# Kernel optimization log

Measured on AMD Instinct MI355X. Metric: run time of the kernel, lower is better.

## Reference

```python
import jax, jax.numpy as jnp
import numpy as np

B, H, D, SIZE, S = 32, 16, 64, 262144, 1024
GAMMA = 0.99

def setup_inputs() -> dict:
    key = jax.random.key(0)
    k1, k2, k3, k4 = jax.random.split(key, 4)
    return {
        "query": jax.random.normal(k1, (B, H, D), jnp.float32),
        "key_store": jax.random.normal(k2, (SIZE, H, D), jnp.float32),
        "value_store": jax.random.normal(k3, (SIZE, H, D), jnp.float32),
        "logit_store": 0.1 * jax.random.normal(k4, (SIZE, H), jnp.float32),
    }

def _sample_indices(logit_store, batch, rng):
    # torch softmax over dim=0 (batch*head rows) => per-row weights over s are
    # w[s] proportional to exp(logit[s,h]) / sum_h' exp(logit[s,h'])
    logw = logit_store.T - jax.nn.logsumexp(logit_store, axis=1)[None, :]  # (H, SIZE)
    u = jax.random.uniform(rng, (batch,) + logw.shape, minval=1e-12, maxval=1.0)
    gumbel = -jnp.log(-jnp.log(u))
    # Gumbel top-k == sampling without replacement proportional to exp(logw)
    _, idx = jax.lax.top_k(logw[None] + gumbel, S)  # (B, H, S)
    return idx

def reference(query, key_store, value_store, logit_store):
    b, h, d = query.shape
    idx = _sample_indices(logit_store, b, jax.random.key(42))  # (B,H,S)
    hidx = jnp.arange(h)[None, :, None]  # (1,H,1) broadcasts against idx
    kst = key_store.transpose(1, 0, 2)   # (H, SIZE, D)
    vst = value_store.transpose(1, 0, 2)
    sk = kst[hidx, idx]  # (B,H,S,D) gathered sample keys
    sv = vst[hidx, idx]  # (B,H,S,D) gathered sample values
    attn = jax.nn.softmax(jnp.einsum('bhd,bhsd->bhs', query, sk) * (d ** -0.5), axis=-1)
    lerp_k = jnp.einsum('bhs,bhsd->bhd', attn, sk)
    lerp_v = jnp.einsum('bhs,bhsd->bhd', attn, sv)
    # scattered in-place store updates
    new_k = (1.0 - attn)[..., None] * sk + attn[..., None] * lerp_k[:, :, None, :]
    new_v = (1.0 - attn)[..., None] * sv + attn[..., None] * lerp_v[:, :, None, :]
    key_store_new = kst.at[hidx, idx].set(new_k).transpose(1, 0, 2)
    value_store_new = vst.at[hidx, idx].set(new_v).transpose(1, 0, 2)
    lst = logit_store.T  # (H, SIZE)
    new_l = GAMMA * lst[hidx, idx] + attn  # RHS uses gathered old logits (matches torch)
    logit_store_new = lst.at[hidx, idx].set(new_l).T
    return lerp_k, lerp_v, key_store_new, value_store_new, logit_store_new
```

## Files before the change

kernel.cpp:

```cpp
#include <hip/hip_runtime.h>
#include <stdint.h>

static constexpr int NB = 32, NH = 16, ND = 64, NS = 1024;
static constexpr int SZ = 262144;
static constexpr int NROW = NB * NH;
static constexpr long N4 = 67108864L;
static constexpr long HALF4 = 33554432L;
static constexpr int SPLIT_IDX = 131072;

typedef float f32x4 __attribute__((ext_vector_type(4)));

__device__ __forceinline__ uint32_t rotl32(uint32_t x, int r) { return (x << r) | (x >> (32 - r)); }

__device__ __forceinline__ void tf2x32(uint32_t x0, uint32_t x1, uint32_t& o0, uint32_t& o1) {
  const uint32_t K1 = 42u, K2 = 0x1BD11BF0u;
  x1 += K1;
#define TFR(r) { x0 += x1; x1 = rotl32(x1, (r)); x1 ^= x0; }
  TFR(13) TFR(15) TFR(26) TFR(6)
  x0 += K1; x1 += K2 + 1u;
  TFR(17) TFR(29) TFR(16) TFR(24)
  x0 += K2; x1 += 2u;
  TFR(13) TFR(15) TFR(26) TFR(6)
  x1 += K1 + 3u;
  TFR(17) TFR(29) TFR(16) TFR(24)
  x0 += K1; x1 += K2 + 4u;
  TFR(13) TFR(15) TFR(26) TFR(6)
  x0 += K2; x1 += 5u;
#undef TFR
  o0 = x0; o1 = x1;
}

__device__ __forceinline__ uint32_t bits_of(uint32_t row, uint32_t s) {
  uint32_t o0, o1; tf2x32(0u, (row << 18) | s, o0, o1);
  return o0 ^ o1;
}

__device__ __forceinline__ float gumbel_precise(uint32_t row, uint32_t s) {
  uint32_t bits = bits_of(row, s);
  float f = __uint_as_float((bits >> 9) | 0x3f800000u) - 1.0f;
  float u = fmaxf(1e-12f, f + 1e-12f);
  float t = -logf(u);
  return -logf(t);
}

__device__ __forceinline__ float uf_of(uint32_t row, uint32_t s) {
  return __uint_as_float((bits_of(row, s) >> 9) | 0x3f800000u);
}

__device__ __forceinline__ uint32_t fkey(float v) {
  uint32_t u = __float_as_uint(v);
  return (u & 0x80000000u) ? ~u : (u | 0x80000000u);
}

__global__ void k_logw(const float* __restrict__ logit, float* __restrict__ logw,
                       float* __restrict__ wexp, float* __restrict__ outL,
                       int* __restrict__ winner, float* __restrict__ W) {
  __shared__ float sW[16];
  const int tid = threadIdx.x;
  if (tid < 16) sW[tid] = 0.f;
  __syncthreads();
  int s = blockIdx.x * 256 + tid;
  const float4* p = (const float4*)(logit + (size_t)s * NH);
  float4 a0 = p[0], a1 = p[1], a2 = p[2], a3 = p[3];
  float x[16] = {a0.x,a0.y,a0.z,a0.w, a1.x,a1.y,a1.z,a1.w,
                 a2.x,a2.y,a2.z,a2.w, a3.x,a3.y,a3.z,a3.w};
  float m = x[0];
#pragma unroll
  for (int h = 1; h < 16; ++h) m = fmaxf(m, x[h]);
  float acc = 0.f;
#pragma unroll
  for (int h = 0; h < 16; ++h) acc += expf(x[h] - m);
  float lse = logf(acc) + m;
  float wl[16];
#pragma unroll
  for (int h = 0; h < 16; ++h) {
    float lw = x[h] - lse;
    logw[(size_t)h * SZ + s] = lw;
    float e = expf(lw);
    wexp[(size_t)h * SZ + s] = e;
    wl[h] = e;
  }
#pragma unroll
  for (int h = 0; h < 16; ++h) {
    float v = wl[h];
#pragma unroll
    for (int off = 32; off; off >>= 1) v += __shfl_xor(v, off);
    if ((tid & 63) == 0) atomicAdd(&sW[h], v);
  }
  float4* q = (float4*)(outL + (size_t)s * NH);
  q[0] = a0; q[1] = a1; q[2] = a2; q[3] = a3;
  int4 mone = make_int4(-1, -1, -1, -1);
  int4* w = (int4*)(winner + (size_t)s * NH);
  w[0] = mone; w[1] = mone; w[2] = mone; w[3] = mone;
  __syncthreads();
  if (tid < 16) atomicAdd(&W[tid], sW[tid]);
}

__device__ __forceinline__ void find_thresh(const uint32_t* hist, int nbins, int chunk,
                                            uint32_t need, int* outT, int tid) {
  if (tid < 64) {
    int hi = nbins - 1 - tid * chunk;
    uint32_t csum = 0;
    for (int j = 0; j < chunk; ++j) csum += hist[hi - j];
    uint32_t inc = csum;
#pragma unroll
    for (int off = 1; off < 64; off <<= 1) {
      uint32_t t = (uint32_t)__shfl_up((int)inc, off);
      if (tid >= off) inc += t;
    }
    uint32_t pre = inc - csum;
    if (pre < need && inc >= need) {
      uint32_t cum = pre; int T = hi - chunk + 1;
      for (int j = 0; j < chunk; ++j) {
        int b = hi - j;
        if (cum + hist[b] >= need) { T = b; break; }
        cum += hist[b];
      }
      *outT = T;
    }
  }
}

#define MEGA_T 512
#define SEL_BLKS 512
#define COPY_BLKS 2048
#define NCAND 5120
__global__ void __launch_bounds__(MEGA_T, 8) k_mega(
    const float* __restrict__ logw, const float* __restrict__ wexp,
    const float* __restrict__ Wsum, const float* __restrict__ qin,
    const float* __restrict__ Kst, const float* __restrict__ Vst,
    int* __restrict__ idx_sel, float* __restrict__ attn_ws,
    float* __restrict__ lerp_k, float* __restrict__ lerp_v, int* __restrict__ winner,
    f32x4* __restrict__ oK4, f32x4* __restrict__ oV4) {
  const int bid = blockIdx.x;
  const int tid = threadIdx.x;

  if (bid >= SEL_BLKS) {
    const f32x4* K4 = (const f32x4*)Kst;
    const f32x4* V4 = (const f32x4*)Vst;
    const long base = (long)(bid - SEL_BLKS) * MEGA_T + tid;
    const long stride = (long)COPY_BLKS * MEGA_T;
    for (int r = 0; r < 8; ++r) {
      long i0 = base + (long)(4 * r) * stride;
      long i1 = i0 + stride, i2 = i0 + 2 * stride, i3 = i0 + 3 * stride;
      f32x4 k0 = __builtin_nontemporal_load(&K4[i0]);
      f32x4 k1 = __builtin_nontemporal_load(&K4[i1]);
      f32x4 k2 = __builtin_nontemporal_load(&K4[i2]);
      f32x4 k3 = __builtin_nontemporal_load(&K4[i3]);
      f32x4 v0 = __builtin_nontemporal_load(&V4[i0]);
      f32x4 v1 = __builtin_nontemporal_load(&V4[i1]);
      f32x4 v2 = __builtin_nontemporal_load(&V4[i2]);
      f32x4 v3 = __builtin_nontemporal_load(&V4[i3]);
      __builtin_nontemporal_store(k0, &oK4[i0]);
      __builtin_nontemporal_store(k1, &oK4[i1]);
      __builtin_nontemporal_store(k2, &oK4[i2]);
      __builtin_nontemporal_store(k3, &oK4[i3]);
      __builtin_nontemporal_store(v0, &oV4[i0]);
      __builtin_nontemporal_store(v1, &oV4[i1]);
      __builtin_nontemporal_store(v2, &oV4[i2]);
      __builtin_nontemporal_store(v3, &oV4[i3]);
    }
    return;
  }

  const int row = bid;
  const int h = row & 15, b = row >> 4;
  const float* lw = logw + (size_t)h * SZ;
  const f32x4* we4 = (const f32x4*)(wexp + (size_t)h * SZ);
  int* outrow = idx_sel + (size_t)row * NS;

  __shared__ union {
    struct {
      int      cidx[NCAND];
      uint32_t hist[2048];
      uint16_t candA[2048];
      uint16_t candB[256];
      uint16_t candC[64];
    } s;
    struct {
      int   sel_s[NS];
      float sc[NS];
      float red[MEGA_T];
      f32x4 pk4[8][16], pv4[8][16];
    } a;
  } u;
  __shared__ int ctl[8];
  __shared__ float sNB;

  if (tid == 0) {
    float Wh = Wsum[h];
    sNB = -4096.0f / Wh;
    ctl[1] = 0;
  }
  __syncthreads();
  const float nB = sNB;
  const float CThr = 1.9999996f;

  for (int g = tid; g < SZ / 4; g += MEGA_T) {
    f32x4 w4 = we4[g];
    int s0 = g << 2;
    float u0 = uf_of(row, s0);
    float u1 = uf_of(row, s0 + 1);
    float u2 = uf_of(row, s0 + 2);
    float u3 = uf_of(row, s0 + 3);
    if (u0 >= fmaf(nB, w4.x, CThr)) { int p = atomicAdd(&ctl[1], 1); if (p < NCAND) u.s.cidx[p] = s0; }
    if (u1 >= fmaf(nB, w4.y, CThr)) { int p = atomicAdd(&ctl[1], 1); if (p < NCAND) u.s.cidx[p] = s0 + 1; }
    if (u2 >= fmaf(nB, w4.z, CThr)) { int p = atomicAdd(&ctl[1], 1); if (p < NCAND) u.s.cidx[p] = s0 + 2; }
    if (u3 >= fmaf(nB, w4.w, CThr)) { int p = atomicAdd(&ctl[1], 1); if (p < NCAND) u.s.cidx[p] = s0 + 3; }
  }
  __syncthreads();
  const int C = min(ctl[1], NCAND);

  for (int i = tid; i < 2048; i += MEGA_T) u.s.hist[i] = 0;
  if (tid == 0) { ctl[0] = 0; ctl[3] = 0; ctl[4] = 0; ctl[5] = 0; }
  __syncthreads();
  for (int ci = tid; ci < C; ci += MEGA_T) {
    int s = u.s.cidx[ci];
    uint32_t k = fkey(lw[s] + gumbel_precise(row, s));
    atomicAdd(&u.s.hist[k >> 21], 1u);
  }
  __syncthreads();
  find_thresh(u.s.hist, 2048, 32, (uint32_t)NS, &ctl[2], tid);
  __syncthreads();
  const int T0 = ctl[2];
  for (int ci = tid; ci < C; ci += MEGA_T) {
    int s = u.s.cidx[ci];
    uint32_t k = fkey(lw[s] + gumbel_precise(row, s));
    int bb = (int)(k >> 21);
    if (bb > T0)       { int p = atomicAdd(&ctl[0], 1); outrow[p] = s; }
    else if (bb == T0) { int c = atomicAdd(&ctl[3], 1); if (c < 2048) u.s.candA[c] = (uint16_t)ci; }
  }
  __syncthreads();
  const int CA = min(ctl[3], 2048);
  for (int i = tid; i < 2048; i += MEGA_T) u.s.hist[i] = 0;
  __syncthreads();
  for (int i = tid; i < CA; i += MEGA_T) {
    int s = u.s.cidx[u.s.candA[i]];
    uint32_t k = fkey(lw[s] + gumbel_precise(row, s));
    atomicAdd(&u.s.hist[(k >> 10) & 0x7FFu], 1u);
  }
  __syncthreads();
  find_thresh(u.s.hist, 2048, 32, (uint32_t)(NS - ctl[0]), &ctl[2], tid);
  __syncthreads();
  const int T1 = ctl[2];
  for (int i = tid; i < CA; i += MEGA_T) {
    int ci = u.s.candA[i];
    int s = u.s.cidx[ci];
    uint32_t k = fkey(lw[s] + gumbel_precise(row, s));
    int mid = (int)((k >> 10) & 0x7FFu);
    if (mid > T1)       { int p = atomicAdd(&ctl[0], 1); outrow[p] = s; }
    else if (mid == T1) { int c = atomicAdd(&ctl[4], 1); if (c < 256) u.s.candB[c] = (uint16_t)ci; }
  }
  __syncthreads();
  const int CB = min(ctl[4], 256);
  for (int i = tid; i < 1024; i += MEGA_T) u.s.hist[i] = 0;
  __syncthreads();
  for (int i = tid; i < CB; i += MEGA_T) {
    int s = u.s.cidx[u.s.candB[i]];
    uint32_t k = fkey(lw[s] + gumbel_precise(row, s));
    atomicAdd(&u.s.hist[k & 0x3FFu], 1u);
  }
  __syncthreads();
  find_thresh(u.s.hist, 1024, 16, (uint32_t)(NS - ctl[0]), &ctl[2], tid);
  __syncthreads();
  const int T2 = ctl[2];
  for (int i = tid; i < CB; i += MEGA_T) {
    int ci = u.s.candB[i];
    int s = u.s.cidx[ci];
    uint32_t k = fkey(lw[s] + gumbel_precise(row, s));
    int lo = (int)(k & 0x3FFu);
    if (lo > T2)       { int p = atomicAdd(&ctl[0], 1); outrow[p] = s; }
    else if (lo == T2) { int c = atomicAdd(&ctl[5], 1); if (c < 64) u.s.candC[c] = (uint16_t)ci; }
  }
  __syncthreads();
  if (tid == 0) {
    int need = NS - ctl[0];
    int cc = min(ctl[5], 64);
    for (int k = 0; k < need; ++k) {
      int best = 0x7fffffff, bi = 0;
      for (int j = 0; j < cc; ++j) { int s = u.s.cidx[u.s.candC[j]]; if (s < best) { best = s; bi = j; } }
      if (best == 0x7fffffff) best = 0;
      outrow[ctl[0] + k] = best;
      if (cc > 0) u.s.cidx[u.s.candC[bi]] = 0x7fffffff;
    }
  }
  __syncthreads();

  const f32x4* K4 = (const f32x4*)Kst;
  const f32x4* V4 = (const f32x4*)Vst;
  const int lane = tid & 63, wv = tid >> 6;
  const int sj = lane >> 3, dj = lane & 7;
  for (int i = tid; i < NS; i += MEGA_T) u.a.sel_s[i] = outrow[i];
  const f32x4* q4 = (const f32x4*)(qin + (size_t)row * ND);
  f32x4 qa = q4[dj * 2], qb = q4[dj * 2 + 1];
  __syncthreads();
  for (int it = 0; it < 16; it += 2) {
    int i1 = it * 64 + wv * 8 + sj;
    int i2 = i1 + 64;
    int x1 = u.a.sel_s[i1], x2 = u.a.sel_s[i2];
    size_t b1 = ((size_t)x1 * NH + h) * 16 + dj * 2;
    size_t b2 = ((size_t)x2 * NH + h) * 16 + dj * 2;
    f32x4 ka1 = K4[b1], kb1 = K4[b1 + 1];
    f32x4 ka2 = K4[b2], kb2 = K4[b2 + 1];
    float p1 = ka1.x*qa.x + ka1.y*qa.y + ka1.z*qa.z + ka1.w*qa.w
             + kb1.x*qb.x + kb1.y*qb.y + kb1.z*qb.z + kb1.w*qb.w;
    float p2 = ka2.x*qa.x + ka2.y*qa.y + ka2.z*qa.z + ka2.w*qa.w
             + kb2.x*qb.x + kb2.y*qb.y + kb2.z*qb.z + kb2.w*qb.w;
#pragma unroll
    for (int off = 1; off < 8; off <<= 1) { p1 += __shfl_xor(p1, off); p2 += __shfl_xor(p2, off); }
    if (dj == 0) { u.a.sc[i1] = p1 * 0.125f; u.a.sc[i2] = p2 * 0.125f; }
  }
  __syncthreads();
  float v1 = u.a.sc[tid], v2 = u.a.sc[tid + 512];
  u.a.red[tid] = fmaxf(v1, v2); __syncthreads();
  for (int s = 256; s; s >>= 1) { if (tid < s) u.a.red[tid] = fmaxf(u.a.red[tid], u.a.red[tid + s]); __syncthreads(); }
  float m = u.a.red[0]; __syncthreads();
  float e1 = expf(v1 - m), e2 = expf(v2 - m);
  u.a.red[tid] = e1 + e2; __syncthreads();
  for (int s = 256; s; s >>= 1) { if (tid < s) u.a.red[tid] += u.a.red[tid + s]; __syncthreads(); }
  float inv = 1.0f / u.a.red[0];
  float a1 = e1 * inv, a2 = e2 * inv;
  u.a.sc[tid] = a1; u.a.sc[tid + 512] = a2;
  attn_ws[(size_t)row * NS + tid] = a1;
  attn_ws[(size_t)row * NS + tid + 512] = a2;
  __syncthreads();
  f32x4 AK = 0.f, BK = 0.f, AV = 0.f, BV = 0.f;
  for (int it = 0; it < 16; it += 2) {
    int i1 = it * 64 + wv * 8 + sj;
    int i2 = i1 + 64;
    int x1 = u.a.sel_s[i1], x2 = u.a.sel_s[i2];
    float c1 = u.a.sc[i1], c2 = u.a.sc[i2];
    size_t b1 = ((size_t)x1 * NH + h) * 16 + dj * 2;
    size_t b2 = ((size_t)x2 * NH + h) * 16 + dj * 2;
    f32x4 k1a = K4[b1], k1b = K4[b1 + 1], v1a = V4[b1], v1b = V4[b1 + 1];
    f32x4 k2a = K4[b2], k2b = K4[b2 + 1], v2a = V4[b2], v2b = V4[b2 + 1];
    AK += c1 * k1a + c2 * k2a; BK += c1 * k1b + c2 * k2b;
    AV += c1 * v1a + c2 * v2a; BV += c1 * v1b + c2 * v2b;
  }
#pragma unroll
  for (int off = 8; off < 64; off <<= 1) {
    AK.x += __shfl_xor(AK.x, off); AK.y += __shfl_xor(AK.y, off);
    AK.z += __shfl_xor(AK.z, off); AK.w += __shfl_xor(AK.w, off);
    BK.x += __shfl_xor(BK.x, off); BK.y += __shfl_xor(BK.y, off);
    BK.z += __shfl_xor(BK.z, off); BK.w += __shfl_xor(BK.w, off);
    AV.x += __shfl_xor(AV.x, off); AV.y += __shfl_xor(AV.y, off);
    AV.z += __shfl_xor(AV.z, off); AV.w += __shfl_xor(AV.w, off);
    BV.x += __shfl_xor(BV.x, off); BV.y += __shfl_xor(BV.y, off);
    BV.z += __shfl_xor(BV.z, off); BV.w += __shfl_xor(BV.w, off);
  }
  if (sj == 0) {
    u.a.pk4[wv][dj * 2] = AK; u.a.pk4[wv][dj * 2 + 1] = BK;
    u.a.pv4[wv][dj * 2] = AV; u.a.pv4[wv][dj * 2 + 1] = BV;
  }
  __syncthreads();
  if (tid < 64) {
    float lk = 0.f, lv = 0.f;
    const float* pkf = (const float*)u.a.pk4;
    const float* pvf = (const float*)u.a.pv4;
#pragma unroll
    for (int ww = 0; ww < 8; ++ww) { lk += pkf[ww * 64 + tid]; lv += pvf[ww * 64 + tid]; }
    lerp_k[(size_t)row * ND + tid] = lk;
    lerp_v[(size_t)row * ND + tid] = lv;
  }
  for (int i = tid; i < NS; i += MEGA_T) atomicMax(&winner[(size_t)u.a.sel_s[i] * NH + h], b);
}

__global__ void k_mark(const int* __restrict__ idx_sel, const float* __restrict__ attn_ws,
                       const int* __restrict__ winner, const float* __restrict__ Lst,
                       float* __restrict__ wa, float* __restrict__ outL) {
  int t = blockIdx.x * 256 + threadIdx.x;
  int row = t >> 10, h = row & 15, b = row >> 4;
  int idx = idx_sel[t];
  size_t slot = (size_t)idx * NH + h;
  if (winner[slot] == b) {
    float a = attn_ws[t];
    wa[slot] = a;
    outL[slot] = 0.99f * Lst[slot] + a;
  }
}

#define TAIL_COPY_BLKS 4096
__global__ void __launch_bounds__(256) k_tail(const f32x4* __restrict__ K4,
    const f32x4* __restrict__ V4, const int* __restrict__ winner,
    const float* __restrict__ wa, const f32x4* __restrict__ LK4,
    const f32x4* __restrict__ LV4, const int* __restrict__ idx_sel,
    const float* __restrict__ attn_ws, f32x4* __restrict__ oK4, f32x4* __restrict__ oV4) {
  const int bid = blockIdx.x;
  if (bid < TAIL_COPY_BLKS) {
    const long base = HALF4 + (long)bid * 256 + threadIdx.x;
    const long stride = (long)TAIL_COPY_BLKS * 256;
    for (int r = 0; r < 8; ++r) {
      long i0 = base + (long)(4 * r) * stride;
      long i1 = i0 + stride, i2 = i0 + 2 * stride, i3 = i0 + 3 * stride;
      int s0 = (int)(i0 >> 4), s1 = (int)(i1 >> 4), s2 = (int)(i2 >> 4), s3 = (int)(i3 >> 4);
      int w0 = winner[s0], w1 = winner[s1], w2 = winner[s2], w3 = winner[s3];
      f32x4 k0 = __builtin_nontemporal_load(&K4[i0]);
      f32x4 k1 = __builtin_nontemporal_load(&K4[i1]);
// ... 47 lines not shown
  float kv = ((const float*)K4)[base], vv = ((const float*)V4)[base];
  float lk = ((const float*)LK4)[(size_t)row * ND + lane];
  float lv = ((const float*)LV4)[(size_t)row * ND + lane];
  float o = 1.0f - a;
  ((float*)oK4)[base] = o * kv + a * lk;
  ((float*)oV4)[base] = o * vv + a * lv;
}

extern "C" void kernel_launch(void* const* d_in, const int* in_sizes, int n_in,
                              void* d_out, int out_size, void* d_ws, size_t ws_size,
                              hipStream_t stream) {
  const float* q   = (const float*)d_in[0];
  const float* Kst = (const float*)d_in[1];
  const float* Vst = (const float*)d_in[2];
  const float* Lst = (const float*)d_in[3];

  float* out    = (float*)d_out;
  float* out_lk = out;
  float* out_lv = out + 32768;
  float* outK   = out + 65536;
  float* outV   = outK + 268435456;
  float* outL   = outV + 268435456;

  char* ws = (char*)d_ws;
  float* logw   = (float*)ws;
  float* wexp   = (float*)(ws + (16ull << 20));
  int*   idxsel = (int*)(ws + (32ull << 20));
  float* attn   = (float*)(ws + (34ull << 20));
  int*   winner = (int*)(ws + (36ull << 20));
  float* wa     = (float*)(ws + (52ull << 20));
  float* Wsum   = (float*)(ws + (68ull << 20));

  hipMemsetAsync(Wsum, 0, 16 * sizeof(float), stream);
  k_logw<<<SZ / 256, 256, 0, stream>>>(Lst, logw, wexp, outL, winner, Wsum);
  k_mega<<<SEL_BLKS + COPY_BLKS, MEGA_T, 0, stream>>>(logw, wexp, Wsum, q, Kst, Vst,
                                                      idxsel, attn, out_lk, out_lv, winner,
                                                      (f32x4*)outK, (f32x4*)outV);
  k_mark<<<NROW * NS / 256, 256, 0, stream>>>(idxsel, attn, winner, Lst, wa, outL);
  k_tail<<<TAIL_COPY_BLKS + NROW * NS / 4, 256, 0, stream>>>(
      (const f32x4*)Kst, (const f32x4*)Vst, winner, wa,
      (const f32x4*)out_lk, (const f32x4*)out_lv, idxsel, attn,
      (f32x4*)outK, (f32x4*)outV);
}
```

Before: 1.172 ms.

## Move part of the store copy into the logw kernel and use single-pass online-softmax attention

```diff
diff --git a/kernel.cpp b/kernel.cpp
--- a/kernel.cpp
+++ b/kernel.cpp
@@ -5,6 +5,7 @@
 static constexpr int SZ = 262144;
 static constexpr int NROW = NB * NH;
 static constexpr long N4 = 67108864L;
+static constexpr long PRE4 = 8388608L;
 static constexpr long HALF4 = 33554432L;
 static constexpr int SPLIT_IDX = 131072;
 
@@ -52,94 +53,18 @@
   return (u & 0x80000000u) ? ~u : (u | 0x80000000u);
 }
 
-__global__ void k_logw(const float* __restrict__ logit, float* __restrict__ logw,
-                       float* __restrict__ wexp, float* __restrict__ outL,
-                       int* __restrict__ winner, float* __restrict__ W) {
-  __shared__ float sW[16];
-  const int tid = threadIdx.x;
-  if (tid < 16) sW[tid] = 0.f;
-  __syncthreads();
-  int s = blockIdx.x * 256 + tid;
-  const float4* p = (const float4*)(logit + (size_t)s * NH);
-  float4 a0 = p[0], a1 = p[1], a2 = p[2], a3 = p[3];
-  float x[16] = {a0.x,a0.y,a0.z,a0.w, a1.x,a1.y,a1.z,a1.w,
-                 a2.x,a2.y,a2.z,a2.w, a3.x,a3.y,a3.z,a3.w};
-  float m = x[0];
-#pragma unroll
-  for (int h = 1; h < 16; ++h) m = fmaxf(m, x[h]);
-  float acc = 0.f;
-#pragma unroll
-  for (int h = 0; h < 16; ++h) acc += expf(x[h] - m);
-  float lse = logf(acc) + m;
-  float wl[16];
-#pragma unroll
-  for (int h = 0; h < 16; ++h) {
-    float lw = x[h] - lse;
-    logw[(size_t)h * SZ + s] = lw;
-    float e = expf(lw);
-    wexp[(size_t)h * SZ + s] = e;
-    wl[h] = e;
-  }
-#pragma unroll
-  for (int h = 0; h < 16; ++h) {
-    float v = wl[h];
-#pragma unroll
-    for (int off = 32; off; off >>= 1) v += __shfl_xor(v, off);
-    if ((tid & 63) == 0) atomicAdd(&sW[h], v);
-  }
-  float4* q = (float4*)(outL + (size_t)s * NH);
-  q[0] = a0; q[1] = a1; q[2] = a2; q[3] = a3;
-  int4 mone = make_int4(-1, -1, -1, -1);
-  int4* w = (int4*)(winner + (size_t)s * NH);
-  w[0] = mone; w[1] = mone; w[2] = mone; w[3] = mone;
-  __syncthreads();
-  if (tid < 16) atomicAdd(&W[tid], sW[tid]);
-}
-
-__device__ __forceinline__ void find_thresh(const uint32_t* hist, int nbins, int chunk,
-                                            uint32_t need, int* outT, int tid) {
-  if (tid < 64) {
-    int hi = nbins - 1 - tid * chunk;
-    uint32_t csum = 0;
-    for (int j = 0; j < chunk; ++j) csum += hist[hi - j];
-    uint32_t inc = csum;
-#pragma unroll
-    for (int off = 1; off < 64; off <<= 1) {
-      uint32_t t = (uint32_t)__shfl_up((int)inc, off);
-      if (tid >= off) inc += t;
-    }
-    uint32_t pre = inc - csum;
-    if (pre < need && inc >= need) {
-      uint32_t cum = pre; int T = hi - chunk + 1;
-      for (int j = 0; j < chunk; ++j) {
-        int b = hi - j;
-        if (cum + hist[b] >= need) { T = b; break; }
-        cum += hist[b];
-      }
-      *outT = T;
-    }
-  }
-}
-
-#define MEGA_T 512
-#define SEL_BLKS 512
-#define COPY_BLKS 2048
-#define NCAND 5120
-__global__ void __launch_bounds__(MEGA_T, 8) k_mega(
-    const float* __restrict__ logw, const float* __restrict__ wexp,
-    const float* __restrict__ Wsum, const float* __restrict__ qin,
-    const float* __restrict__ Kst, const float* __restrict__ Vst,
-    int* __restrict__ idx_sel, float* __restrict__ attn_ws,
-    float* __restrict__ lerp_k, float* __restrict__ lerp_v, int* __restrict__ winner,
+#define PRE_LOGW_BLKS 1024
+#define PRE_COPY_BLKS 1024
+__global__ void __launch_bounds__(256) k_pre(const float* __restrict__ logit,
+    float* __restrict__ logw, float* __restrict__ wexp, float* __restrict__ outL,
+    int* __restrict__ winner, float* __restrict__ W,
+    const f32x4* __restrict__ K4, const f32x4* __restrict__ V4,
     f32x4* __restrict__ oK4, f32x4* __restrict__ oV4) {
   const int bid = blockIdx.x;
   const int tid = threadIdx.x;
-
-  if (bid >= SEL_BLKS) {
-    const f32x4* K4 = (const f32x4*)Kst;
-    const f32x4* V4 = (const f32x4*)Vst;
-    const long base = (long)(bid - SEL_BLKS) * MEGA_T + tid;
-    const long stride = (long)COPY_BLKS * MEGA_T;
+  if (bid >= PRE_LOGW_BLKS) {
+    const long base = (long)(bid - PRE_LOGW_BLKS) * 256 + tid;
+    const long stride = (long)PRE_COPY_BLKS * 256;
     for (int r = 0; r < 8; ++r) {
       long i0 = base + (long)(4 * r) * stride;
       long i1 = i0 + stride, i2 = i0 + 2 * stride, i3 = i0 + 3 * stride;
@@ -162,6 +87,112 @@
     }
     return;
   }
+  __shared__ float sW[16];
+  if (tid < 16) sW[tid] = 0.f;
+  __syncthreads();
+  int s = bid * 256 + tid;
+  const float4* p = (const float4*)(logit + (size_t)s * NH);
+  float4 a0 = p[0], a1 = p[1], a2 = p[2], a3 = p[3];
+  float x[16] = {a0.x,a0.y,a0.z,a0.w, a1.x,a1.y,a1.z,a1.w,
+                 a2.x,a2.y,a2.z,a2.w, a3.x,a3.y,a3.z,a3.w};
+  float m = x[0];
+#pragma unroll
+  for (int h = 1; h < 16; ++h) m = fmaxf(m, x[h]);
+  float acc = 0.f;
+#pragma unroll
+  for (int h = 0; h < 16; ++h) acc += expf(x[h] - m);
+  float lse = logf(acc) + m;
+  float wl[16];
+#pragma unroll
+  for (int h = 0; h < 16; ++h) {
+    float lw = x[h] - lse;
+    logw[(size_t)h * SZ + s] = lw;
+    float e = expf(lw);
+    wexp[(size_t)h * SZ + s] = e;
+    wl[h] = e;
+  }
+#pragma unroll
+  for (int h = 0; h < 16; ++h) {
+    float v = wl[h];
+#pragma unroll
+    for (int off = 32; off; off >>= 1) v += __shfl_xor(v, off);
+    if ((tid & 63) == 0) atomicAdd(&sW[h], v);
+  }
+  float4* q = (float4*)(outL + (size_t)s * NH);
+  q[0] = a0; q[1] = a1; q[2] = a2; q[3] = a3;
+  int4 mone = make_int4(-1, -1, -1, -1);
+  int4* w = (int4*)(winner + (size_t)s * NH);
+  w[0] = mone; w[1] = mone; w[2] = mone; w[3] = mone;
+  __syncthreads();
+  if (tid < 16) atomicAdd(&W[tid], sW[tid]);
+}
+
+__device__ __forceinline__ void find_thresh(const uint32_t* hist, int nbins, int chunk,
+                                            uint32_t need, int* outT, int tid) {
+  if (tid < 64) {
+    int hi = nbins - 1 - tid * chunk;
+    uint32_t csum = 0;
+    for (int j = 0; j < chunk; ++j) csum += hist[hi - j];
+    uint32_t inc = csum;
+#pragma unroll
+    for (int off = 1; off < 64; off <<= 1) {
+      uint32_t t = (uint32_t)__shfl_up((int)inc, off);
+      if (tid >= off) inc += t;
+    }
+    uint32_t pre = inc - csum;
+    if (pre < need && inc >= need) {
+      uint32_t cum = pre; int T = hi - chunk + 1;
+      for (int j = 0; j < chunk; ++j) {
+        int b = hi - j;
+        if (cum + hist[b] >= need) { T = b; break; }
+        cum += hist[b];
+      }
+      *outT = T;
+    }
+  }
+}
+
+#define MEGA_T 512
+#define SEL_BLKS 512
+#define COPY_BLKS 2048
+#define NCAND 5120
+__global__ void __launch_bounds__(MEGA_T, 8) k_mega(
+    const float* __restrict__ logw, const float* __restrict__ wexp,
+    const float* __restrict__ Wsum, const float* __restrict__ qin,
+    const float* __restrict__ Kst, const float* __restrict__ Vst,
+    int* __restrict__ idx_sel, float* __restrict__ attn_ws,
+    float* __restrict__ lerp_k, float* __restrict__ lerp_v, int* __restrict__ winner,
+    f32x4* __restrict__ oK4, f32x4* __restrict__ oV4) {
+  const int bid = blockIdx.x;
+  const int tid = threadIdx.x;
+
+  if (bid >= SEL_BLKS) {
+    const f32x4* K4 = (const f32x4*)Kst;
+    const f32x4* V4 = (const f32x4*)Vst;
+    const long base = PRE4 + (long)(bid - SEL_BLKS) * MEGA_T + tid;
+    const long stride = (long)COPY_BLKS * MEGA_T;
+    for (int r = 0; r < 6; ++r) {
+      long i0 = base + (long)(4 * r) * stride;
+      long i1 = i0 + stride, i2 = i0 + 2 * stride, i3 = i0 + 3 * stride;
+      f32x4 k0 = __builtin_nontemporal_load(&K4[i0]);
+      f32x4 k1 = __builtin_nontemporal_load(&K4[i1]);
+      f32x4 k2 = __builtin_nontemporal_load(&K4[i2]);
+      f32x4 k3 = __builtin_nontemporal_load(&K4[i3]);
+      f32x4 v0 = __builtin_nontemporal_load(&V4[i0]);
+      f32x4 v1 = __builtin_nontemporal_load(&V4[i1]);
+      f32x4 v2 = __builtin_nontemporal_load(&V4[i2]);
+      f32x4 v3 = __builtin_nontemporal_load(&V4[i3]);
+      __builtin_nontemporal_store(k0, &oK4[i0]);
+      __builtin_nontemporal_store(k1, &oK4[i1]);
+      __builtin_nontemporal_store(k2, &oK4[i2]);
+      __builtin_nontemporal_store(k3, &oK4[i3]);
+      __builtin_nontemporal_store(v0, &oV4[i0]);
+      __builtin_nontemporal_store(v1, &oV4[i1]);
+      __builtin_nontemporal_store(v2, &oV4[i2]);
+      __builtin_nontemporal_store(v3, &oV4[i3]);
+    }
+    return;
+  }
 
   const int row = bid;
   const int h = row & 15, b = row >> 4;
@@ -180,8 +211,8 @@
     struct {
       int   sel_s[NS];
       float sc[NS];
-      float red[MEGA_T];
       f32x4 pk4[8][16], pv4[8][16];
+      float mw[8], lw8[8], mL[2];
     } a;
   } u;
   __shared__ int ctl[8];
@@ -294,74 +325,78 @@
   const f32x4* q4 = (const f32x4*)(qin + (size_t)row * ND);
   f32x4 qa = q4[dj * 2], qb = q4[dj * 2 + 1];
   __syncthreads();
-  for (int it = 0; it < 16; it += 2) {
+  float mg = -1e30f, lg = 0.f;
+  f32x4 AK = 0.f, BK = 0.f, AV = 0.f, BV = 0.f;
+  for (int it = 0; it < 16; ++it) {
     int i1 = it * 64 + wv * 8 + sj;
-    int i2 = i1 + 64;
-    int x1 = u.a.sel_s[i1], x2 = u.a.sel_s[i2];
+    int x1 = u.a.sel_s[i1];
     size_t b1 = ((size_t)x1 * NH + h) * 16 + dj * 2;
-    size_t b2 = ((size_t)x2 * NH + h) * 16 + dj * 2;
-    f32x4 ka1 = K4[b1], kb1 = K4[b1 + 1];
-    f32x4 ka2 = K4[b2], kb2 = K4[b2 + 1];
-    float p1 = ka1.x*qa.x + ka1.y*qa.y + ka1.z*qa.z + ka1.w*qa.w
-             + kb1.x*qb.x + kb1.y*qb.y + kb1.z*qb.z + kb1.w*qb.w;
-    float p2 = ka2.x*qa.x + ka2.y*qa.y + ka2.z*qa.z + ka2.w*qa.w
-             + kb2.x*qb.x + kb2.y*qb.y + kb2.z*qb.z + kb2.w*qb.w;
-#pragma unroll
-    for (int off = 1; off < 8; off <<= 1) { p1 += __shfl_xor(p1, off); p2 += __shfl_xor(p2, off); }
-    if (dj == 0) { u.a.sc[i1] = p1 * 0.125f; u.a.sc[i2] = p2 * 0.125f; }
-  }
-  __syncthreads();
-  float v1 = u.a.sc[tid], v2 = u.a.sc[tid + 512];
-  u.a.red[tid] = fmaxf(v1, v2); __syncthreads();
-  for (int s = 256; s; s >>= 1) { if (tid < s) u.a.red[tid] = fmaxf(u.a.red[tid], u.a.red[tid + s]); __syncthreads(); }
-  float m = u.a.red[0]; __syncthreads();
-  float e1 = expf(v1 - m), e2 = expf(v2 - m);
-  u.a.red[tid] = e1 + e2; __syncthreads();
-  for (int s = 256; s; s >>= 1) { if (tid < s) u.a.red[tid] += u.a.red[tid + s]; __syncthreads(); }
-  float inv = 1.0f / u.a.red[0];
-  float a1 = e1 * inv, a2 = e2 * inv;
-  u.a.sc[tid] = a1; u.a.sc[tid + 512] = a2;
-  attn_ws[(size_t)row * NS + tid] = a1;
-  attn_ws[(size_t)row * NS + tid + 512] = a2;
-  __syncthreads();
-  f32x4 AK = 0.f, BK = 0.f, AV = 0.f, BV = 0.f;
-  for (int it = 0; it < 16; it += 2) {
-    int i1 = it * 64 + wv * 8 + sj;
-    int i2 = i1 + 64;
-    int x1 = u.a.sel_s[i1], x2 = u.a.sel_s[i2];
-    float c1 = u.a.sc[i1], c2 = u.a.sc[i2];
-    size_t b1 = ((size_t)x1 * NH + h) * 16 + dj * 2;
-    size_t b2 = ((size_t)x2 * NH + h) * 16 + dj * 2;
-    f32x4 k1a = K4[b1], k1b = K4[b1 + 1], v1a = V4[b1], v1b = V4[b1 + 1];
-    f32x4 k2a = K4[b2], k2b = K4[b2 + 1], v2a = V4[b2], v2b = V4[b2 + 1];
-    AK += c1 * k1a + c2 * k2a; BK += c1 * k1b + c2 * k2b;
-    AV += c1 * v1a + c2 * v2a; BV += c1 * v1b + c2 * v2b;
+    f32x4 ka = K4[b1], kb = K4[b1 + 1];
+    f32x4 va = V4[b1], vb = V4[b1 + 1];
+    float p = ka.x*qa.x + ka.y*qa.y + ka.z*qa.z + ka.w*qa.w
+            + kb.x*qb.x + kb.y*qb.y + kb.z*qb.z + kb.w*qb.w;
+#pragma unroll
+    for (int off = 1; off < 8; off <<= 1) p += __shfl_xor(p, off);
+    p *= 0.125f;
+    if (dj == 0) u.a.sc[i1] = p;
+    float mn = fmaxf(mg, p);
+    float sca = expf(mg - mn);
+    float pe  = expf(p - mn);
+    lg = lg * sca + pe;
+    AK = AK * sca + pe * ka; BK = BK * sca + pe * kb;
+    AV = AV * sca + pe * va; BV = BV * sca + pe * vb;
+    mg = mn;
   }
 #pragma unroll
   for (int off = 8; off < 64; off <<= 1) {
-    AK.x += __shfl_xor(AK.x, off); AK.y += __shfl_xor(AK.y, off);
-    AK.z += __shfl_xor(AK.z, off); AK.w += __shfl_xor(AK.w, off);
-    BK.x += __shfl_xor(BK.x, off); BK.y += __shfl_xor(BK.y, off);
-    BK.z += __shfl_xor(BK.z, off); BK.w += __shfl_xor(BK.w, off);
-    AV.x += __shfl_xor(AV.x, off); AV.y += __shfl_xor(AV.y, off);
-    AV.z += __shfl_xor(AV.z, off); AV.w += __shfl_xor(AV.w, off);
-    BV.x += __shfl_xor(BV.x, off); BV.y += __shfl_xor(BV.y, off);
-    BV.z += __shfl_xor(BV.z, off); BV.w += __shfl_xor(BV.w, off);
+    float mo = __shfl_xor(mg, off);
+    float lo = __shfl_xor(lg, off);
+    f32x4 tAK, tBK, tAV, tBV;
+    tAK.x = __shfl_xor(AK.x, off); tAK.y = __shfl_xor(AK.y, off);
+    tAK.z = __shfl_xor(AK.z, off); tAK.w = __shfl_xor(AK.w, off);
+    tBK.x = __shfl_xor(BK.x, off); tBK.y = __shfl_xor(BK.y, off);
+    tBK.z = __shfl_xor(BK.z, off); tBK.w = __shfl_xor(BK.w, off);
+    tAV.x = __shfl_xor(AV.x, off); tAV.y = __shfl_xor(AV.y, off);
+    tAV.z = __shfl_xor(AV.z, off); tAV.w = __shfl_xor(AV.w, off);
+    tBV.x = __shfl_xor(BV.x, off); tBV.y = __shfl_xor(BV.y, off);
+    tBV.z = __shfl_xor(BV.z, off); tBV.w = __shfl_xor(BV.w, off);
+    float mn = fmaxf(mg, mo);
+    float s1 = expf(mg - mn), s2 = expf(mo - mn);
+    lg = lg * s1 + lo * s2;
+    AK = AK * s1 + tAK * s2; BK = BK * s1 + tBK * s2;
+    AV = AV * s1 + tAV * s2; BV = BV * s1 + tBV * s2;
+    mg = mn;
   }
   if (sj == 0) {
     u.a.pk4[wv][dj * 2] = AK; u.a.pk4[wv][dj * 2 + 1] = BK;
     u.a.pv4[wv][dj * 2] = AV; u.a.pv4[wv][dj * 2 + 1] = BV;
   }
+  if (lane == 0) { u.a.mw[wv] = mg; u.a.lw8[wv] = lg; }
   __syncthreads();
   if (tid < 64) {
-    float lk = 0.f, lv = 0.f;
+    float m = -1e30f;
+#pragma unroll
+    for (int w = 0; w < 8; ++w) m = fmaxf(m, u.a.mw[w]);
+    float L = 0.f, lk = 0.f, lv = 0.f;
     const float* pkf = (const float*)u.a.pk4;
     const float* pvf = (const float*)u.a.pv4;
 #pragma unroll
-    for (int ww = 0; ww < 8; ++ww) { lk += pkf[ww * 64 + tid]; lv += pvf[ww * 64 + tid]; }
-    lerp_k[(size_t)row * ND + tid] = lk;
-    lerp_v[(size_t)row * ND + tid] = lv;
-  }
+    for (int w = 0; w < 8; ++w) {
+      float f = expf(u.a.mw[w] - m);
+      L  += u.a.lw8[w] * f;
+      lk += pkf[w * 64 + tid] * f;
+      lv += pvf[w * 64 + tid] * f;
+    }
+    lerp_k[(size_t)row * ND + tid] = lk / L;
+    lerp_v[(size_t)row * ND + tid] = lv / L;
+    if (tid == 0) { u.a.mL[0] = m; u.a.mL[1] = L; }
+  }
+  __syncthreads();
+  const float gm = u.a.mL[0], gLinv = 1.0f / u.a.mL[1];
+  float a1 = expf(u.a.sc[tid] - gm) * gLinv;
+  float a2 = expf(u.a.sc[tid + 512] - gm) * gLinv;
+  attn_ws[(size_t)row * NS + tid] = a1;
+  attn_ws[(size_t)row * NS + tid + 512] = a2;
   for (int i = tid; i < NS; i += MEGA_T) atomicMax(&winner[(size_t)u.a.sel_s[i] * NH + h], b);
 }
 
@@ -476,7 +511,9 @@
   float* Wsum   = (float*)(ws + (68ull << 20));
 
   hipMemsetAsync(Wsum, 0, 16 * sizeof(float), stream);
-  k_logw<<<SZ / 256, 256, 0, stream>>>(Lst, logw, wexp, outL, winner, Wsum);
+  k_pre<<<PRE_LOGW_BLKS + PRE_COPY_BLKS, 256, 0, stream>>>(
+      Lst, logw, wexp, outL, winner, Wsum,
+      (const f32x4*)Kst, (const f32x4*)Vst, (f32x4*)outK, (f32x4*)outV);
   k_mega<<<SEL_BLKS + COPY_BLKS, MEGA_T, 0, stream>>>(logw, wexp, Wsum, q, Kst, Vst,
                                                       idxsel, attn, out_lk, out_lv, winner,
                                                       (f32x4*)outK, (f32x4*)outV);
```

Result: slower. 1.294 ms (+10.4%).

## Split fused select/attention kernel into two kernels sharing the bulk store copy

Applied to the files above, without the earlier changes.

```diff
diff --git a/kernel.cpp b/kernel.cpp
--- a/kernel.cpp
+++ b/kernel.cpp
@@ -5,6 +5,7 @@
 static constexpr int SZ = 262144;
 static constexpr int NROW = NB * NH;
 static constexpr long N4 = 67108864L;
+static constexpr long Q38 = 25165824L;
 static constexpr long HALF4 = 33554432L;
 static constexpr int SPLIT_IDX = 131072;
 
@@ -121,16 +122,14 @@
   }
 }
 
-#define MEGA_T 512
+#define SEL_T 512
 #define SEL_BLKS 512
-#define COPY_BLKS 2048
+#define WCOPY_BLKS 2048
 #define NCAND 5120
-__global__ void __launch_bounds__(MEGA_T, 8) k_mega(
+__global__ void __launch_bounds__(SEL_T, 8) k_sel(
     const float* __restrict__ logw, const float* __restrict__ wexp,
-    const float* __restrict__ Wsum, const float* __restrict__ qin,
-    const float* __restrict__ Kst, const float* __restrict__ Vst,
-    int* __restrict__ idx_sel, float* __restrict__ attn_ws,
-    float* __restrict__ lerp_k, float* __restrict__ lerp_v, int* __restrict__ winner,
+    const float* __restrict__ Wsum, const float* __restrict__ Kst,
+    const float* __restrict__ Vst, int* __restrict__ idx_sel,
     f32x4* __restrict__ oK4, f32x4* __restrict__ oV4) {
   const int bid = blockIdx.x;
   const int tid = threadIdx.x;
@@ -138,9 +137,9 @@
   if (bid >= SEL_BLKS) {
     const f32x4* K4 = (const f32x4*)Kst;
     const f32x4* V4 = (const f32x4*)Vst;
-    const long base = (long)(bid - SEL_BLKS) * MEGA_T + tid;
-    const long stride = (long)COPY_BLKS * MEGA_T;
-    for (int r = 0; r < 8; ++r) {
+    const long base = (long)(bid - SEL_BLKS) * SEL_T + tid;
+    const long stride = (long)WCOPY_BLKS * SEL_T;
+    for (int r = 0; r < 6; ++r) {
       long i0 = base + (long)(4 * r) * stride;
       long i1 = i0 + stride, i2 = i0 + 2 * stride, i3 = i0 + 3 * stride;
       f32x4 k0 = __builtin_nontemporal_load(&K4[i0]);
@@ -164,26 +163,16 @@
   }
 
   const int row = bid;
-  const int h = row & 15, b = row >> 4;
+  const int h = row & 15;
   const float* lw = logw + (size_t)h * SZ;
   const f32x4* we4 = (const f32x4*)(wexp + (size_t)h * SZ);
   int* outrow = idx_sel + (size_t)row * NS;
 
-  __shared__ union {
-    struct {
-      int      cidx[NCAND];
-      uint32_t hist[2048];
-      uint16_t candA[2048];
-      uint16_t candB[256];
-      uint16_t candC[64];
-    } s;
-    struct {
-      int   sel_s[NS];
-      float sc[NS];
-      float red[MEGA_T];
-      f32x4 pk4[8][16], pv4[8][16];
-    } a;
-  } u;
+  __shared__ int      cidx[NCAND];
+  __shared__ uint32_t hist[2048];
+  __shared__ uint16_t candA[2048];
+  __shared__ uint16_t candB[256];
+  __shared__ uint16_t candC[64];
   __shared__ int ctl[8];
   __shared__ float sNB;
 
@@ -196,81 +185,86 @@
   const float nB = sNB;
   const float CThr = 1.9999996f;
 
-  for (int g = tid; g < SZ / 4; g += MEGA_T) {
-    f32x4 w4 = we4[g];
-    int s0 = g << 2;
-    float u0 = uf_of(row, s0);
-    float u1 = uf_of(row, s0 + 1);
-    float u2 = uf_of(row, s0 + 2);
-    float u3 = uf_of(row, s0 + 3);
-    if (u0 >= fmaf(nB, w4.x, CThr)) { int p = atomicAdd(&ctl[1], 1); if (p < NCAND) u.s.cidx[p] = s0; }
-    if (u1 >= fmaf(nB, w4.y, CThr)) { int p = atomicAdd(&ctl[1], 1); if (p < NCAND) u.s.cidx[p] = s0 + 1; }
-    if (u2 >= fmaf(nB, w4.z, CThr)) { int p = atomicAdd(&ctl[1], 1); if (p < NCAND) u.s.cidx[p] = s0 + 2; }
-    if (u3 >= fmaf(nB, w4.w, CThr)) { int p = atomicAdd(&ctl[1], 1); if (p < NCAND) u.s.cidx[p] = s0 + 3; }
+  {
+    f32x4 w4 = we4[tid];
+    for (int g = tid; g < SZ / 4; g += SEL_T) {
+      f32x4 wc = w4;
+      int gn = g + SEL_T;
+      if (gn < SZ / 4) w4 = we4[gn];
+      int s0 = g << 2;
+      float u0 = uf_of(row, s0);
+      float u1 = uf_of(row, s0 + 1);
+      float u2 = uf_of(row, s0 + 2);
+      float u3 = uf_of(row, s0 + 3);
+      if (u0 >= fmaf(nB, wc.x, CThr)) { int p = atomicAdd(&ctl[1], 1); if (p < NCAND) cidx[p] = s0; }
+      if (u1 >= fmaf(nB, wc.y, CThr)) { int p = atomicAdd(&ctl[1], 1); if (p < NCAND) cidx[p] = s0 + 1; }
+      if (u2 >= fmaf(nB, wc.z, CThr)) { int p = atomicAdd(&ctl[1], 1); if (p < NCAND) cidx[p] = s0 + 2; }
+      if (u3 >= fmaf(nB, wc.w, CThr)) { int p = atomicAdd(&ctl[1], 1); if (p < NCAND) cidx[p] = s0 + 3; }
+    }
   }
   __syncthreads();
   const int C = min(ctl[1], NCAND);
 
-  for (int i = tid; i < 2048; i += MEGA_T) u.s.hist[i] = 0;
+  for (int i = tid; i < 2048; i += SEL_T) hist[i] = 0;
   if (tid == 0) { ctl[0] = 0; ctl[3] = 0; ctl[4] = 0; ctl[5] = 0; }
   __syncthreads();
-  for (int ci = tid; ci < C; ci += MEGA_T) {
-    int s = u.s.cidx[ci];
+  for (int ci = tid; ci < C; ci += SEL_T) {
+    int s = cidx[ci];
     uint32_t k = fkey(lw[s] + gumbel_precise(row, s));
-    atomicAdd(&u.s.hist[k >> 21], 1u);
-  }
-  __syncthreads();
-  find_thresh(u.s.hist, 2048, 32, (uint32_t)NS, &ctl[2], tid);
+    atomicAdd(&hist[k >> 21], 1u);
+  }
+  __syncthreads();
+  find_thresh(hist, 2048, 32, (uint32_t)NS, &ctl[2], tid);
   __syncthreads();
   const int T0 = ctl[2];
-  for (int ci = tid; ci < C; ci += MEGA_T) {
-    int s = u.s.cidx[ci];
+  for (int ci = tid; ci < C; ci += SEL_T) {
+    int s = cidx[ci];
     uint32_t k = fkey(lw[s] + gumbel_precise(row, s));
     int bb = (int)(k >> 21);
     if (bb > T0)       { int p = atomicAdd(&ctl[0], 1); outrow[p] = s; }
-    else if (bb == T0) { int c = atomicAdd(&ctl[3], 1); if (c < 2048) u.s.candA[c] = (uint16_t)ci; }
+    else if (bb == T0) { int c = atomicAdd(&ctl[3], 1); if (c < 2048) candA[c] = (uint16_t)ci; }
   }
   __syncthreads();
   const int CA = min(ctl[3], 2048);
-  for (int i = tid; i < 2048; i += MEGA_T) u.s.hist[i] = 0;
-  __syncthreads();
-  for (int i = tid; i < CA; i += MEGA_T) {
-    int s = u.s.cidx[u.s.candA[i]];
+  for (int i = tid; i < 2048; i += SEL_T) hist[i] = 0;
+  __syncthreads();
+  for (int i = tid; i < CA; i += SEL_T) {
+    int s = cidx[candA[i]];
     uint32_t k = fkey(lw[s] + gumbel_precise(row, s));
-    atomicAdd(&u.s.hist[(k >> 10) & 0x7FFu], 1u);
-  }
-  __syncthreads();
-  find_thresh(u.s.hist, 2048, 32, (uint32_t)(NS - ctl[0]), &ctl[2], tid);
+    atomicAdd(&hist[(k >> 10) & 0x7FFu], 1u);
+  }
+  __syncthreads();
+  find_thresh(hist, 2048, 32, (uint32_t)(NS - ctl[0]), &ctl[2], tid);
   __syncthreads();
   const int T1 = ctl[2];
-  for (int i = tid; i < CA; i += MEGA_T) {
-    int ci = u.s.candA[i];
-    int s = u.s.cidx[ci];
+  for (int i = tid; i < CA; i += SEL_T) {
+    int ci = candA[i];
+    int s = cidx[ci];
     uint32_t k = fkey(lw[s] + gumbel_precise(row, s));
     int mid = (int)((k >> 10) & 0x7FFu);
     if (mid > T1)       { int p = atomicAdd(&ctl[0], 1); outrow[p] = s; }
-    else if (mid == T1) { int c = atomicAdd(&ctl[4], 1); if (c < 256) u.s.candB[c] = (uint16_t)ci; }
+    else if (mid == T1) { int c = atomicAdd(&ctl[4], 1); if (c < 256) candB[c] = (uint16_t)ci; }
   }
   __syncthreads();
   const int CB = min(ctl[4], 256);
-  for (int i = tid; i < 1024; i += MEGA_T) u.s.hist[i] = 0;
-  __syncthreads();
-  for (int i = tid; i < CB; i += MEGA_T) {
-    int s = u.s.cidx[u.s.candB[i]];
+  for (int i = tid; i < 1024; i += SEL_T) hist[i] = 0;
+  __syncthreads();
+  for (int i = tid; i < CB; i += SEL_T) {
+    int s = cidx[candB[i]];
     uint32_t k = fkey(lw[s] + gumbel_precise(row, s));
-    atomicAdd(&u.s.hist[k & 0x3FFu], 1u);
-  }
-  __syncthreads();
-  find_thresh(u.s.hist, 1024, 16, (uint32_t)(NS - ctl[0]), &ctl[2], tid);
+    atomicAdd(&hist[k & 0x3FFu], 1u);
+  }
+  __syncthreads();
+  find_thresh(hist, 1024, 16, (uint32_t)(NS - ctl[0]), &ctl[2], tid);
   __syncthreads();
   const int T2 = ctl[2];
-  for (int i = tid; i < CB; i += MEGA_T) {
-    int ci = u.s.candB[i];
-    int s = u.s.cidx[ci];
+  for (int i = tid; i < CB; i += SEL_T) {
+    int ci = candB[i];
+    int s = cidx[ci];
     uint32_t k = fkey(lw[s] + gumbel_precise(row, s));
     int lo = (int)(k & 0x3FFu);
     if (lo > T2)       { int p = atomicAdd(&ctl[0], 1); outrow[p] = s; }
-    else if (lo == T2) { int c = atomicAdd(&ctl[5], 1); if (c < 64) u.s.candC[c] = (uint16_t)ci; }
+    else if (lo == T2) { int c = atomicAdd(&ctl[5], 1); if (c < 64) candC[c] = (uint16_t)ci; }
   }
   __syncthreads();
   if (tid == 0) {
@@ -278,26 +272,68 @@
     int cc = min(ctl[5], 64);
     for (int k = 0; k < need; ++k) {
       int best = 0x7fffffff, bi = 0;
-      for (int j = 0; j < cc; ++j) { int s = u.s.cidx[u.s.candC[j]]; if (s < best) { best = s; bi = j; } }
+      for (int j = 0; j < cc; ++j) { int s = cidx[candC[j]]; if (s < best) { best = s; bi = j; } }
       if (best == 0x7fffffff) best = 0;
       outrow[ctl[0] + k] = best;
-      if (cc > 0) u.s.cidx[u.s.candC[bi]] = 0x7fffffff;
-    }
-  }
-  __syncthreads();
-
+      if (cc > 0) cidx[candC[bi]] = 0x7fffffff;
+    }
+  }
+}
+
+__global__ void __launch_bounds__(SEL_T, 8) k_attn(
+    const float* __restrict__ qin, const float* __restrict__ Kst,
+    const float* __restrict__ Vst, const int* __restrict__ idx_sel,
+    float* __restrict__ attn_ws, float* __restrict__ lerp_k,
+    float* __restrict__ lerp_v, int* __restrict__ winner,
+    f32x4* __restrict__ oK4, f32x4* __restrict__ oV4) {
+  const int bid = blockIdx.x;
+  const int tid = threadIdx.x;
   const f32x4* K4 = (const f32x4*)Kst;
   const f32x4* V4 = (const f32x4*)Vst;
+
+  if (bid >= SEL_BLKS) {
+    const long base = Q38 + (long)(bid - SEL_BLKS) * SEL_T + tid;
+    const long stride = (long)WCOPY_BLKS * SEL_T;
+    for (int r = 0; r < 2; ++r) {
+      long i0 = base + (long)(4 * r) * stride;
+      long i1 = i0 + stride, i2 = i0 + 2 * stride, i3 = i0 + 3 * stride;
+      f32x4 k0 = __builtin_nontemporal_load(&K4[i0]);
+      f32x4 k1 = __builtin_nontemporal_load(&K4[i1]);
+      f32x4 k2 = __builtin_nontemporal_load(&K4[i2]);
+      f32x4 k3 = __builtin_nontemporal_load(&K4[i3]);
+      f32x4 v0 = __builtin_nontemporal_load(&V4[i0]);
+      f32x4 v1 = __builtin_nontemporal_load(&V4[i1]);
+      f32x4 v2 = __builtin_nontemporal_load(&V4[i2]);
+      f32x4 v3 = __builtin_nontemporal_load(&V4[i3]);
+      __builtin_nontemporal_store(k0, &oK4[i0]);
+      __builtin_nontemporal_store(k1, &oK4[i1]);
+      __builtin_nontemporal_store(k2, &oK4[i2]);
+      __builtin_nontemporal_store(k3, &oK4[i3]);
+      __builtin_nontemporal_store(v0, &oV4[i0]);
+      __builtin_nontemporal_store(v1, &oV4[i1]);
+      __builtin_nontemporal_store(v2, &oV4[i2]);
+      __builtin_nontemporal_store(v3, &oV4[i3]);
+    }
+    return;
+  }
+
+  const int row = bid;
+  const int h = row & 15, b = row >> 4;
   const int lane = tid & 63, wv = tid >> 6;
   const int sj = lane >> 3, dj = lane & 7;
-  for (int i = tid; i < NS; i += MEGA_T) u.a.sel_s[i] = outrow[i];
+  __shared__ int   sel_s[NS];
+  __shared__ float sc[NS];
+  __shared__ float red[SEL_T];
+  __shared__ f32x4 pk4[8][16], pv4[8][16];
+  const int* sel = idx_sel + (size_t)row * NS;
+  for (int i = tid; i < NS; i += SEL_T) sel_s[i] = sel[i];
   const f32x4* q4 = (const f32x4*)(qin + (size_t)row * ND);
   f32x4 qa = q4[dj * 2], qb = q4[dj * 2 + 1];
   __syncthreads();
   for (int it = 0; it < 16; it += 2) {
     int i1 = it * 64 + wv * 8 + sj;
     int i2 = i1 + 64;
-    int x1 = u.a.sel_s[i1], x2 = u.a.sel_s[i2];
+    int x1 = sel_s[i1], x2 = sel_s[i2];
     size_t b1 = ((size_t)x1 * NH + h) * 16 + dj * 2;
     size_t b2 = ((size_t)x2 * NH + h) * 16 + dj * 2;
     f32x4 ka1 = K4[b1], kb1 = K4[b1 + 1];
@@ -308,19 +344,19 @@
              + kb2.x*qb.x + kb2.y*qb.y + kb2.z*qb.z + kb2.w*qb.w;
 #pragma unroll
     for (int off = 1; off < 8; off <<= 1) { p1 += __shfl_xor(p1, off); p2 += __shfl_xor(p2, off); }
-    if (dj == 0) { u.a.sc[i1] = p1 * 0.125f; u.a.sc[i2] = p2 * 0.125f; }
-  }
-  __syncthreads();
-  float v1 = u.a.sc[tid], v2 = u.a.sc[tid + 512];
-  u.a.red[tid] = fmaxf(v1, v2); __syncthreads();
-  for (int s = 256; s; s >>= 1) { if (tid < s) u.a.red[tid] = fmaxf(u.a.red[tid], u.a.red[tid + s]); __syncthreads(); }
-  float m = u.a.red[0]; __syncthreads();
+    if (dj == 0) { sc[i1] = p1 * 0.125f; sc[i2] = p2 * 0.125f; }
+  }
+  __syncthreads();
+  float v1 = sc[tid], v2 = sc[tid + 512];
+  red[tid] = fmaxf(v1, v2); __syncthreads();
+  for (int s = 256; s; s >>= 1) { if (tid < s) red[tid] = fmaxf(red[tid], red[tid + s]); __syncthreads(); }
+  float m = red[0]; __syncthreads();
   float e1 = expf(v1 - m), e2 = expf(v2 - m);
-  u.a.red[tid] = e1 + e2; __syncthreads();
-  for (int s = 256; s; s >>= 1) { if (tid < s) u.a.red[tid] += u.a.red[tid + s]; __syncthreads(); }
-  float inv = 1.0f / u.a.red[0];
+  red[tid] = e1 + e2; __syncthreads();
+  for (int s = 256; s; s >>= 1) { if (tid < s) red[tid] += red[tid + s]; __syncthreads(); }
+  float inv = 1.0f / red[0];
   float a1 = e1 * inv, a2 = e2 * inv;
-  u.a.sc[tid] = a1; u.a.sc[tid + 512] = a2;
+  sc[tid] = a1; sc[tid + 512] = a2;
   attn_ws[(size_t)row * NS + tid] = a1;
   attn_ws[(size_t)row * NS + tid + 512] = a2;
   __syncthreads();
@@ -328,8 +364,8 @@
   for (int it = 0; it < 16; it += 2) {
     int i1 = it * 64 + wv * 8 + sj;
     int i2 = i1 + 64;
-    int x1 = u.a.sel_s[i1], x2 = u.a.sel_s[i2];
-    float c1 = u.a.sc[i1], c2 = u.a.sc[i2];
+    int x1 = sel_s[i1], x2 = sel_s[i2];
+    float c1 = sc[i1], c2 = sc[i2];
     size_t b1 = ((size_t)x1 * NH + h) * 16 + dj * 2;
     size_t b2 = ((size_t)x2 * NH + h) * 16 + dj * 2;
     f32x4 k1a = K4[b1], k1b = K4[b1 + 1], v1a = V4[b1], v1b = V4[b1 + 1];
@@ -349,20 +385,20 @@
     BV.z += __shfl_xor(BV.z, off); BV.w += __shfl_xor(BV.w, off);
   }
   if (sj == 0) {
-    u.a.pk4[wv][dj * 2] = AK; u.a.pk4[wv][dj * 2 + 1] = BK;
-    u.a.pv4[wv][dj * 2] = AV; u.a.pv4[wv][dj * 2 + 1] = BV;
+    pk4[wv][dj * 2] = AK; pk4[wv][dj * 2 + 1] = BK;
+    pv4[wv][dj * 2] = AV; pv4[wv][dj * 2 + 1] = BV;
   }
   __syncthreads();
   if (tid < 64) {
     float lk = 0.f, lv = 0.f;
-    const float* pkf = (const float*)u.a.pk4;
-    const float* pvf = (const float*)u.a.pv4;
+    const float* pkf = (const float*)pk4;
+    const float* pvf = (const float*)pv4;
 #pragma unroll
     for (int ww = 0; ww < 8; ++ww) { lk += pkf[ww * 64 + tid]; lv += pvf[ww * 64 + tid]; }
     lerp_k[(size_t)row * ND + tid] = lk;
     lerp_v[(size_t)row * ND + tid] = lv;
   }
-  for (int i = tid; i < NS; i += MEGA_T) atomicMax(&winner[(size_t)u.a.sel_s[i] * NH + h], b);
+  for (int i = tid; i < NS; i += SEL_T) atomicMax(&winner[(size_t)sel_s[i] * NH + h], b);
 }
 
 __global__ void k_mark(const int* __restrict__ idx_sel, const float* __restrict__ attn_ws,
@@ -477,8 +513,10 @@
 
   hipMemsetAsync(Wsum, 0, 16 * sizeof(float), stream);
   k_logw<<<SZ / 256, 256, 0, stream>>>(Lst, logw, wexp, outL, winner, Wsum);
-  k_mega<<<SEL_BLKS + COPY_BLKS, MEGA_T, 0, stream>>>(logw, wexp, Wsum, q, Kst, Vst,
-                                                      idxsel, attn, out_lk, out_lv, winner,
+  k_sel<<<SEL_BLKS + WCOPY_BLKS, SEL_T, 0, stream>>>(logw, wexp, Wsum, Kst, Vst, idxsel,
+                                                     (f32x4*)outK, (f32x4*)outV);
+  k_attn<<<SEL_BLKS + WCOPY_BLKS, SEL_T, 0, stream>>>(q, Kst, Vst, idxsel, attn,
+                                                      out_lk, out_lv, winner,
                                                       (f32x4*)outK, (f32x4*)outV);
   k_mark<<<NROW * NS / 256, 256, 0, stream>>>(idxsel, attn, winner, Lst, wa, outL);
   k_tail<<<TAIL_COPY_BLKS + NROW * NS / 4, 256, 0, stream>>>(
```

New measurement: 1.229 ms. +4.8%, slower.

## Move first chunk of K/V store copy into logw kernel to overlap with it

Applied to the files above, without the earlier changes.

```diff
diff --git a/kernel.cpp b/kernel.cpp
--- a/kernel.cpp
+++ b/kernel.cpp
@@ -5,6 +5,7 @@
 static constexpr int SZ = 262144;
 static constexpr int NROW = NB * NH;
 static constexpr long N4 = 67108864L;
+static constexpr long PRE4 = 8388608L;
 static constexpr long HALF4 = 33554432L;
 static constexpr int SPLIT_IDX = 131072;
 
@@ -52,14 +53,44 @@
   return (u & 0x80000000u) ? ~u : (u | 0x80000000u);
 }
 
-__global__ void k_logw(const float* __restrict__ logit, float* __restrict__ logw,
-                       float* __restrict__ wexp, float* __restrict__ outL,
-                       int* __restrict__ winner, float* __restrict__ W) {
+#define PRE_LOGW_BLKS 1024
+#define PRE_COPY_BLKS 1024
+__global__ void __launch_bounds__(256) k_pre(const float* __restrict__ logit,
+    float* __restrict__ logw, float* __restrict__ wexp, float* __restrict__ outL,
+    int* __restrict__ winner, float* __restrict__ W,
+    const f32x4* __restrict__ K4, const f32x4* __restrict__ V4,
+    f32x4* __restrict__ oK4, f32x4* __restrict__ oV4) {
+  const int bid = blockIdx.x;
+  const int tid = threadIdx.x;
+  if (bid >= PRE_LOGW_BLKS) {
+    const long base = (long)(bid - PRE_LOGW_BLKS) * 256 + tid;
+    const long stride = (long)PRE_COPY_BLKS * 256;
+    for (int r = 0; r < 8; ++r) {
+      long i0 = base + (long)(4 * r) * stride;
+      long i1 = i0 + stride, i2 = i0 + 2 * stride, i3 = i0 + 3 * stride;
+      f32x4 k0 = __builtin_nontemporal_load(&K4[i0]);
+      f32x4 k1 = __builtin_nontemporal_load(&K4[i1]);
+      f32x4 k2 = __builtin_nontemporal_load(&K4[i2]);
+      f32x4 k3 = __builtin_nontemporal_load(&K4[i3]);
+      f32x4 v0 = __builtin_nontemporal_load(&V4[i0]);
+      f32x4 v1 = __builtin_nontemporal_load(&V4[i1]);
+      f32x4 v2 = __builtin_nontemporal_load(&V4[i2]);
+      f32x4 v3 = __builtin_nontemporal_load(&V4[i3]);
+      __builtin_nontemporal_store(k0, &oK4[i0]);
+      __builtin_nontemporal_store(k1, &oK4[i1]);
+      __builtin_nontemporal_store(k2, &oK4[i2]);
+      __builtin_nontemporal_store(k3, &oK4[i3]);
+      __builtin_nontemporal_store(v0, &oV4[i0]);
+      __builtin_nontemporal_store(v1, &oV4[i1]);
+      __builtin_nontemporal_store(v2, &oV4[i2]);
+      __builtin_nontemporal_store(v3, &oV4[i3]);
+    }
+    return;
+  }
   __shared__ float sW[16];
-  const int tid = threadIdx.x;
   if (tid < 16) sW[tid] = 0.f;
   __syncthreads();
-  int s = blockIdx.x * 256 + tid;
+  int s = bid * 256 + tid;
   const float4* p = (const float4*)(logit + (size_t)s * NH);
   float4 a0 = p[0], a1 = p[1], a2 = p[2], a3 = p[3];
   float x[16] = {a0.x,a0.y,a0.z,a0.w, a1.x,a1.y,a1.z,a1.w,
@@ -138,9 +169,9 @@
   if (bid >= SEL_BLKS) {
     const f32x4* K4 = (const f32x4*)Kst;
     const f32x4* V4 = (const f32x4*)Vst;
-    const long base = (long)(bid - SEL_BLKS) * MEGA_T + tid;
+    const long base = PRE4 + (long)(bid - SEL_BLKS) * MEGA_T + tid;
     const long stride = (long)COPY_BLKS * MEGA_T;
-    for (int r = 0; r < 8; ++r) {
+    for (int r = 0; r < 6; ++r) {
       long i0 = base + (long)(4 * r) * stride;
       long i1 = i0 + stride, i2 = i0 + 2 * stride, i3 = i0 + 3 * stride;
       f32x4 k0 = __builtin_nontemporal_load(&K4[i0]);
@@ -476,7 +507,9 @@
   float* Wsum   = (float*)(ws + (68ull << 20));
 
   hipMemsetAsync(Wsum, 0, 16 * sizeof(float), stream);
-  k_logw<<<SZ / 256, 256, 0, stream>>>(Lst, logw, wexp, outL, winner, Wsum);
+  k_pre<<<PRE_LOGW_BLKS + PRE_COPY_BLKS, 256, 0, stream>>>(
+      Lst, logw, wexp, outL, winner, Wsum,
+      (const f32x4*)Kst, (const f32x4*)Vst, (f32x4*)outK, (f32x4*)outV);
   k_mega<<<SEL_BLKS + COPY_BLKS, MEGA_T, 0, stream>>>(logw, wexp, Wsum, q, Kst, Vst,
                                                       idxsel, attn, out_lk, out_lv, winner,
                                                       (f32x4*)outK, (f32x4*)outV);
```

Result: slower. 1.208 ms (+3.0%).
